# Optimization experiments

Measured on AMD Instinct MI355X. Metric: run time of the kernel, lower is better.

## Reference

```python
import jax, jax.numpy as jnp
import numpy as np


def setup_inputs() -> dict:
    key = jax.random.key(0)
    ks = jax.random.split(key, 8)
    N, C, H, W = 4, 128, 64, 64
    x = jax.random.normal(ks[0], (N, C, H, W), dtype=jnp.float32)
    s = 1.0 / np.sqrt(C)
    wq = jax.random.normal(ks[1], (C, C), dtype=jnp.float32) * s
    bq = jax.random.normal(ks[2], (C,), dtype=jnp.float32) * 0.01
    wk = jax.random.normal(ks[3], (C, C), dtype=jnp.float32) * s
    bk = jax.random.normal(ks[4], (C,), dtype=jnp.float32) * 0.01
    wv = jax.random.normal(ks[5], (C, C), dtype=jnp.float32) * s
    bv = jax.random.normal(ks[6], (C,), dtype=jnp.float32) * 0.01
    gamma = jax.random.normal(ks[7], (1,), dtype=jnp.float32) * 0.1
    return {"x": x, "wq": wq, "bq": bq, "wk": wk, "bk": bk,
            "wv": wv, "bv": bv, "gamma": gamma}


def reference(x, wq, bq, wk, bk, wv, bv, gamma):
    N, C, H, W = x.shape
    xf = x.reshape(N, C, H * W)                      # [N, C, HW]
    # 1x1 convs == per-pixel channel GEMMs
    q = jnp.einsum('dc,nci->ndi', wq, xf) + bq[None, :, None]  # [N, C, HW]
    k = jnp.einsum('dc,nci->ndi', wk, xf) + bk[None, :, None]
    v = jnp.einsum('dc,nci->ndi', wv, xf) + bv[None, :, None]
    # scores[n,i,j] = sum_c q[n,c,i] * k[n,c,j]  (query^T @ key)
    scores = jnp.einsum('nci,ncj->nij', q, k)        # [N, HW, HW]
    attn = jax.nn.softmax(scores, axis=-1)
    # out[n,c,i] = sum_j v[n,c,j] * attn[n,i,j]  (value @ attn^T)
    out = jnp.einsum('ncj,nij->nci', v, attn).reshape(N, C, H, W)
    return gamma[0] * out + x
```

## Files before the change

kernel.cpp:

```cpp
#include <hip/hip_runtime.h>

#define HW 4096
#define CC 128
#define NSPLIT 4
#define KEYS_PER_SPLIT (HW / NSPLIT)
#define LOG2E 1.44269504088896f

typedef __bf16 bf16x8 __attribute__((ext_vector_type(8)));
typedef __bf16 bf16x4 __attribute__((ext_vector_type(4)));
typedef __bf16 bf16x2 __attribute__((ext_vector_type(2)));
typedef float floatx4 __attribute__((ext_vector_type(4)));

__global__ __launch_bounds__(256) void wconv_kernel(
    const float* __restrict__ wq, const float* __restrict__ wk,
    const float* __restrict__ wv, __bf16* __restrict__ wb)
{
    int idx = blockIdx.x * 256 + threadIdx.x;
    int which = idx >> 14;
    int within = idx & 16383;
    const float* src = (which == 0) ? wq : (which == 1) ? wk : wv;
    wb[idx] = (__bf16)src[within];
}

#define XT_STRIDE 136
#define VT2_STRIDE 40

__global__ __launch_bounds__(256, 4) void proj_kernel(
    const float* __restrict__ x, const __bf16* __restrict__ wb,
    const float* __restrict__ bq, const float* __restrict__ bk,
    const float* __restrict__ bv,
    __bf16* __restrict__ qb, __bf16* __restrict__ kb, __bf16* __restrict__ vb)
{
    __shared__ char smem_raw[128 * VT2_STRIDE * 2];
    __bf16* Xt = reinterpret_cast<__bf16*>(smem_raw);
    __bf16* Vt = reinterpret_cast<__bf16*>(smem_raw);

    const int m   = blockIdx.x % 3;
    const int nit = blockIdx.x / 3;
    const int n   = nit >> 7;
    const int it  = nit & 127;
    const int i0  = it << 5;
    const int t   = threadIdx.x;

    const float* xb = x + (size_t)n * CC * HW;

    {
        const int f = t & 7;
        const int cb = t >> 3;
#pragma unroll
        for (int p = 0; p < 4; ++p) {
            int c = p * 32 + cb;
            float4 xv = *reinterpret_cast<const float4*>(&xb[(size_t)c * HW + i0 + f * 4]);
            Xt[(f * 4 + 0) * XT_STRIDE + c] = (__bf16)xv.x;
            Xt[(f * 4 + 1) * XT_STRIDE + c] = (__bf16)xv.y;
            Xt[(f * 4 + 2) * XT_STRIDE + c] = (__bf16)xv.z;
            Xt[(f * 4 + 3) * XT_STRIDE + c] = (__bf16)xv.w;
        }
    }
    __syncthreads();

    const int w    = t >> 6;
    const int lane = t & 63;
    const int l16  = lane & 15;
    const int quad = lane >> 4;
    const int d0   = w * 32;

    bf16x8 afrag[2][4];
#pragma unroll
    for (int it16 = 0; it16 < 2; ++it16)
#pragma unroll
        for (int ks = 0; ks < 4; ++ks)
            afrag[it16][ks] = *reinterpret_cast<const bf16x8*>(
                &Xt[(it16 * 16 + l16) * XT_STRIDE + ks * 32 + quad * 8]);

    const __bf16* wm = wb + (size_t)m * CC * CC;
    const float* Bm = (m == 0) ? bq : (m == 1) ? bk : bv;
    const float scale = (m == 0) ? LOG2E : 1.0f;

    floatx4 acc[2][2];
#pragma unroll
    for (int dt = 0; dt < 2; ++dt) {
        int d = d0 + dt * 16 + l16;
        bf16x8 bfrag[4];
#pragma unroll
        for (int ks = 0; ks < 4; ++ks)
            bfrag[ks] = *reinterpret_cast<const bf16x8*>(
                wm + (size_t)d * CC + ks * 32 + quad * 8);
#pragma unroll
        for (int it16 = 0; it16 < 2; ++it16) {
            acc[dt][it16] = (floatx4){0.f, 0.f, 0.f, 0.f};
#pragma unroll
            for (int ks = 0; ks < 4; ++ks)
                acc[dt][it16] = __builtin_amdgcn_mfma_f32_16x16x32_bf16(
                    afrag[it16][ks], bfrag[ks], acc[dt][it16], 0, 0, 0);
        }
    }

    if (m < 2) {
        __bf16* dst = (m == 0) ? qb : kb;
#pragma unroll
        for (int dt = 0; dt < 2; ++dt) {
            int d = d0 + dt * 16 + l16;
            float bias = Bm[d];
#pragma unroll
            for (int it16 = 0; it16 < 2; ++it16)
#pragma unroll
                for (int r = 0; r < 4; ++r) {
                    int i = i0 + it16 * 16 + quad * 4 + r;
                    dst[((size_t)n * HW + i) * CC + d] =
                        (__bf16)((acc[dt][it16][r] + bias) * scale);
                }
        }
    } else {
        __syncthreads();
#pragma unroll
        for (int dt = 0; dt < 2; ++dt) {
            int d = d0 + dt * 16 + l16;
            float bias = Bm[d];
#pragma unroll
            for (int it16 = 0; it16 < 2; ++it16)
#pragma unroll
                for (int r = 0; r < 4; ++r)
                    Vt[d * VT2_STRIDE + it16 * 16 + quad * 4 + r] =
                        (__bf16)(acc[dt][it16][r] + bias);
        }
        __syncthreads();
        {
            int d = t >> 1, half = t & 1;
            bf16x8 v0 = *reinterpret_cast<const bf16x8*>(&Vt[d * VT2_STRIDE + half * 16]);
            bf16x8 v1 = *reinterpret_cast<const bf16x8*>(&Vt[d * VT2_STRIDE + half * 16 + 8]);
            __bf16* vp = vb + ((size_t)n * CC + d) * HW + i0 + half * 16;
            *reinterpret_cast<bf16x8*>(vp)     = v0;
            *reinterpret_cast<bf16x8*>(vp + 8) = v1;
        }
    }
}

#define KT_STRIDE 136
#define KT_BYTES (64 * KT_STRIDE * 2)
#define VT_STRIDE 72
#define VT_BYTES (128 * VT_STRIDE * 2)
#define P_OFF    (KT_BYTES + VT_BYTES)
#define PT_STRIDE 72
#define PT_WAVE (32 * PT_STRIDE * 2)
#define T_STRIDE 65

__global__ __launch_bounds__(256, 2) void attn_split_kernel(
    const __bf16* __restrict__ qb, const __bf16* __restrict__ kb,
    const __bf16* __restrict__ vb,
    __bf16* __restrict__ opart, float* __restrict__ ml)
{
    __shared__ char smem[P_OFF + 4 * PT_WAVE];
    __bf16* Kt = reinterpret_cast<__bf16*>(smem);
    __bf16* Vt = reinterpret_cast<__bf16*>(smem + KT_BYTES);
    float*  T  = reinterpret_cast<float*>(smem);

    const int b     = blockIdx.x;
    const int n     = (b >> 1) & 3;
    const int split = (((b >> 3) & 1) << 1) | (b & 1);
    const int it    = b >> 4;
    const int i0    = it << 7;
    const int t     = threadIdx.x;
    const int w     = t >> 6;
    const int lane  = t & 63;
    const int l16   = lane & 15;
    const int quad  = lane >> 4;

    __bf16* Pt = reinterpret_cast<__bf16*>(smem + P_OFF) + w * (32 * PT_STRIDE);

    bf16x8 qfrag[2][4];
#pragma unroll
    for (int half = 0; half < 2; ++half) {
        const __bf16* qrow = qb + ((size_t)n * HW + i0 + w * 32 + half * 16 + l16) * CC;
#pragma unroll
        for (int ks = 0; ks < 4; ++ks)
            qfrag[half][ks] = *reinterpret_cast<const bf16x8*>(qrow + ks * 32 + quad * 8);
    }

    float m_i[2] = {-1e30f, -1e30f};
    float l_i[2] = {0.f, 0.f};
    floatx4 o_acc[2][8];
#pragma unroll
    for (int half = 0; half < 2; ++half)
#pragma unroll
        for (int h = 0; h < 8; ++h) o_acc[half][h] = (floatx4){0.f, 0.f, 0.f, 0.f};

    const __bf16* kbase = kb + (size_t)n * HW * CC;
    const __bf16* vbase = vb + (size_t)n * CC * HW;

    const int jbeg = split * KEYS_PER_SPLIT;
    const int jend = jbeg + KEYS_PER_SPLIT;

    const int jr = t >> 4, ch = t & 15;
    const int cv = t >> 3, ch2 = t & 7;

    for (int j0 = jbeg; j0 < jend; j0 += 64) {
        bf16x8 kst[4], vst[4];
#pragma unroll
        for (int p = 0; p < 4; ++p) {
            kst[p] = *reinterpret_cast<const bf16x8*>(
                kbase + (size_t)(j0 + p * 16 + jr) * CC + ch * 8);
            vst[p] = *reinterpret_cast<const bf16x8*>(
                vbase + (size_t)(p * 32 + cv) * HW + j0 + ch2 * 8);
        }
        __syncthreads();
#pragma unroll
        for (int p = 0; p < 4; ++p) {
            *reinterpret_cast<bf16x8*>(&Kt[(p * 16 + jr) * KT_STRIDE + ch * 8]) = kst[p];
            *reinterpret_cast<bf16x8*>(&Vt[(p * 32 + cv) * VT_STRIDE + ch2 * 8]) = vst[p];
        }
        __syncthreads();

        floatx4 s[2][4];
#pragma unroll
        for (int half = 0; half < 2; ++half)
#pragma unroll
            for (int g = 0; g < 4; ++g) s[half][g] = (floatx4){0.f, 0.f, 0.f, 0.f};
#pragma unroll
        for (int ks = 0; ks < 4; ++ks) {
#pragma unroll
            for (int g = 0; g < 4; ++g) {
                bf16x8 kf = *reinterpret_cast<const bf16x8*>(
                    &Kt[(g * 16 + l16) * KT_STRIDE + ks * 32 + quad * 8]);
                s[0][g] = __builtin_amdgcn_mfma_f32_16x16x32_bf16(kf, qfrag[0][ks], s[0][g], 0, 0, 0);
                s[1][g] = __builtin_amdgcn_mfma_f32_16x16x32_bf16(kf, qfrag[1][ks], s[1][g], 0, 0, 0);
            }
        }

#pragma unroll
        for (int half = 0; half < 2; ++half) {
            float rm = fmaxf(fmaxf(fmaxf(s[half][0][0], s[half][0][1]),
                                   fmaxf(s[half][0][2], s[half][0][3])),
                             fmaxf(fmaxf(s[half][1][0], s[half][1][1]),
                                   fmaxf(s[half][1][2], s[half][1][3])));
            float rm2 = fmaxf(fmaxf(fmaxf(s[half][2][0], s[half][2][1]),
                                    fmaxf(s[half][2][2], s[half][2][3])),
                              fmaxf(fmaxf(s[half][3][0], s[half][3][1]),
                                    fmaxf(s[half][3][2], s[half][3][3])));
            rm = fmaxf(rm, rm2);
            rm = fmaxf(rm, __shfl_xor(rm, 16, 64));
            rm = fmaxf(rm, __shfl_xor(rm, 32, 64));
            if (__any(rm > m_i[half])) {
                float mn = fmaxf(m_i[half], rm);
                float alpha = exp2f(m_i[half] - mn);
                m_i[half] = mn;
                l_i[half] *= alpha;
#pragma unroll
                for (int h = 0; h < 8; ++h)
                    o_acc[half][h] *= alpha;
            }
            float mi = m_i[half];
            float rs = 0.f;
#pragma unroll
            for (int g = 0; g < 4; ++g)
#pragma unroll
                for (int r = 0; r < 4; ++r) {
                    float e = exp2f(s[half][g][r] - mi);
                    s[half][g][r] = e;
                    rs += e;
                }
            rs += __shfl_xor(rs, 16, 64);
            rs += __shfl_xor(rs, 32, 64);
            l_i[half] += rs;

#pragma unroll
            for (int g = 0; g < 4; ++g) {
                bf16x4 pk = {(__bf16)s[half][g][0], (__bf16)s[half][g][1],
                             (__bf16)s[half][g][2], (__bf16)s[half][g][3]};
                *reinterpret_cast<bf16x4*>(
                    &Pt[(half * 16 + l16) * PT_STRIDE + g * 16 + quad * 4]) = pk;
            }
        }

#pragma unroll
        for (int tt = 0; tt < 2; ++tt) {
            bf16x8 pf0 = *reinterpret_cast<const bf16x8*>(
                &Pt[l16 * PT_STRIDE + tt * 32 + quad * 8]);
            bf16x8 pf1 = *reinterpret_cast<const bf16x8*>(
                &Pt[(16 + l16) * PT_STRIDE + tt * 32 + quad * 8]);
#pragma unroll
            for (int h = 0; h < 8; ++h) {
                bf16x8 vf = *reinterpret_cast<const bf16x8*>(
                    &Vt[(h * 16 + l16) * VT_STRIDE + tt * 32 + quad * 8]);
                o_acc[0][h] = __builtin_amdgcn_mfma_f32_16x16x32_bf16(vf, pf0, o_acc[0][h], 0, 0, 0);
                o_acc[1][h] = __builtin_amdgcn_mfma_f32_16x16x32_bf16(vf, pf1, o_acc[1][h], 0, 0, 0);
            }
        }
    }

    if (quad == 0) {
#pragma unroll
        for (int half = 0; half < 2; ++half) {
            int q = w * 32 + half * 16 + l16;
            ml[(size_t)b * 256 + q]       = m_i[half];
            ml[(size_t)b * 256 + 128 + q] = l_i[half];
        }
    }

    float inv[2] = {1.f / l_i[0], 1.f / l_i[1]};

    __syncthreads();
#pragma unroll
    for (int pass = 0; pass < 2; ++pass) {
        if ((w >> 1) == pass) {
            int ql = (w & 1) * 32;
#pragma unroll
            for (int half = 0; half < 2; ++half)
#pragma unroll
                for (int h = 0; h < 8; ++h)
#pragma unroll
                    for (int r = 0; r < 4; ++r)
                        T[(h * 16 + quad * 4 + r) * T_STRIDE + ql + half * 16 + l16] =
                            o_acc[half][h][r] * inv[half];
        }
        __syncthreads();
#pragma unroll 4
        for (int p = 0; p < 16; ++p) {
            int c  = p * 8 + (t >> 5);
            int q2 = (t & 31) * 2;
            float f0 = T[c * T_STRIDE + q2];
            float f1 = T[c * T_STRIDE + q2 + 1];
            bf16x2 pk = {(__bf16)f0, (__bf16)f1};
            *reinterpret_cast<bf16x2*>(
                &opart[(size_t)b * 16384 + (size_t)c * 128 + pass * 64 + q2]) = pk;
        }
        __syncthreads();
    }
}

__global__ __launch_bounds__(256) void combine_kernel(
    const __bf16* __restrict__ opart, const float* __restrict__ ml,
    const float* __restrict__ x, const float* __restrict__ gamma,
    float* __restrict__ out)
{
    __shared__ float wsc[NSPLIT][128];

    const int b2    = blockIdx.x;
    const int cpart = b2 & 7;
    const int qt    = b2 >> 3;
    const int n     = qt >> 5;
    const int it    = qt & 31;
    const int i0    = it << 7;
    const int t     = threadIdx.x;
    const float gm  = gamma[0];

    int battn[NSPLIT];
#pragma unroll
    for (int s = 0; s < NSPLIT; ++s)
        battn[s] = (it << 4) | ((s >> 1) << 3) | (n << 1) | (s & 1);

    if (t < 128) {
        float ms[NSPLIT], ls[NSPLIT], M = -1e30f;
#pragma unroll
        for (int s = 0; s < NSPLIT; ++s) {
            ms[s] = ml[(size_t)battn[s] * 256 + t];
            ls[s] = ml[(size_t)battn[s] * 256 + 128 + t];
            M = fmaxf(M, ms[s]);
        }
        float denom = 0.f, es[NSPLIT];
#pragma unroll
        for (int s = 0; s < NSPLIT; ++s) {
            es[s] = exp2f(ms[s] - M);
            denom += es[s] * ls[s];
        }
        float inv = gm / denom;
#pragma unroll
        for (int s = 0; s < NSPLIT; ++s)
            wsc[s][t] = es[s] * inv;
    }
    __syncthreads();

#pragma unroll
    for (int p = 0; p < 4; ++p) {
        int c  = cpart * 16 + p * 4 + (t >> 6);
        int q2 = (t & 63) * 2;
        size_t gidx = ((size_t)n * CC + c) * HW + i0 + q2;
        float2 xv = *reinterpret_cast<const float2*>(&x[gidx]);
        float a0 = xv.x, a1 = xv.y;
#pragma unroll
        for (int s = 0; s < NSPLIT; ++s) {
            bf16x2 ov = *reinterpret_cast<const bf16x2*>(
                &opart[(size_t)battn[s] * 16384 + (size_t)c * 128 + q2]);
            a0 += wsc[s][q2]     * (float)ov[0];
            a1 += wsc[s][q2 + 1] * (float)ov[1];
        }
        float2 o2 = {a0, a1};
        *reinterpret_cast<float2*>(&out[gidx]) = o2;
    }
}

extern "C" void kernel_launch(void* const* d_in, const int* in_sizes, int n_in,
                              void* d_out, int out_size, void* d_ws, size_t ws_size,
                              hipStream_t stream) {
    const float* x     = (const float*)d_in[0];
    const float* wq    = (const float*)d_in[1];
    const float* bq    = (const float*)d_in[2];
    const float* wk    = (const float*)d_in[3];
    const float* bk    = (const float*)d_in[4];
    const float* wv    = (const float*)d_in[5];
    const float* bv    = (const float*)d_in[6];
    const float* gamma = (const float*)d_in[7];
    float* out = (float*)d_out;

    char* ws = (char*)d_ws;
    const size_t qkv_sz = (size_t)4 * HW * CC * sizeof(__bf16);
    __bf16* qb = (__bf16*)(ws);
    __bf16* kb = (__bf16*)(ws + qkv_sz);
    __bf16* vb = (__bf16*)(ws + 2 * qkv_sz);
    __bf16* wb = (__bf16*)(ws + 3 * qkv_sz);
    __bf16* opart = (__bf16*)(ws + 3 * qkv_sz + 3 * CC * CC * sizeof(__bf16));
    float* ml = (float*)((char*)opart + (size_t)512 * 16384 * sizeof(__bf16));

    wconv_kernel<<<192, 256, 0, stream>>>(wq, wk, wv, wb);
    proj_kernel<<<1536, 256, 0, stream>>>(x, wb, bq, bk, bv, qb, kb, vb);
    attn_split_kernel<<<512, 256, 0, stream>>>(qb, kb, vb, opart, ml);
    combine_kernel<<<1024, 256, 0, stream>>>(opart, ml, x, gamma, out);
}
```

Measured before the change: 144.6 us.

## Stage K/V tiles via direct global-to-LDS DMA with double-buffered V and XOR swizzle

The attention loop now copies K and V tiles straight from global memory into LDS with global_load_lds, so they no longer pass through registers. V is double-buffered and K is prefetched once the score MFMAs finish, which overlaps the loads of the next tile with compute on the current one. Padded LDS strides are replaced by XOR-swizzled layouts for K, V and the per-wave P tile to avoid bank conflicts. The risk is that the DMA path needs correct swizzle and synchronisation, and the K prefetch can still stall on the barrier placed mid-iteration.

```diff
diff --git a/kernel.cpp b/kernel.cpp
--- a/kernel.cpp
+++ b/kernel.cpp
@@ -3,13 +3,21 @@
 #define HW 4096
 #define CC 128
 #define NSPLIT 4
-#define KEYS_PER_SPLIT (HW / NSPLIT)
+#define KPS (HW / NSPLIT)
+#define NJ (KPS / 64)
 #define LOG2E 1.44269504088896f
 
 typedef __bf16 bf16x8 __attribute__((ext_vector_type(8)));
 typedef __bf16 bf16x4 __attribute__((ext_vector_type(4)));
 typedef __bf16 bf16x2 __attribute__((ext_vector_type(2)));
 typedef float floatx4 __attribute__((ext_vector_type(4)));
+
+#define AS1 __attribute__((address_space(1)))
+#define AS3 __attribute__((address_space(3)))
+
+__device__ __forceinline__ void dma16(const __bf16* g, char* l) {
+    __builtin_amdgcn_global_load_lds((const AS1 void*)g, (AS3 void*)l, 16, 0, 0);
+}
 
 __global__ __launch_bounds__(256) void wconv_kernel(
     const float* __restrict__ wq, const float* __restrict__ wk,
@@ -38,19 +46,17 @@
     const int m   = blockIdx.x % 3;
     const int nit = blockIdx.x / 3;
     const int n   = nit >> 7;
-    const int it  = nit & 127;
-    const int i0  = it << 5;
+    const int i0  = (nit & 127) << 5;
     const int t   = threadIdx.x;
 
     const float* xb = x + (size_t)n * CC * HW;
 
     {
-        const int f = t & 7;
-        const int cb = t >> 3;
+        const int f = t & 7, cb = t >> 3;
 #pragma unroll
         for (int p = 0; p < 4; ++p) {
             int c = p * 32 + cb;
-            float4 xv = *reinterpret_cast<const float4*>(&xb[(size_t)c * HW + i0 + f * 4]);
+            float4 xv = *(const float4*)(&xb[(size_t)c * HW + i0 + f * 4]);
             Xt[(f * 4 + 0) * XT_STRIDE + c] = (__bf16)xv.x;
             Xt[(f * 4 + 1) * XT_STRIDE + c] = (__bf16)xv.y;
             Xt[(f * 4 + 2) * XT_STRIDE + c] = (__bf16)xv.z;
@@ -70,7 +76,7 @@
     for (int it16 = 0; it16 < 2; ++it16)
 #pragma unroll
         for (int ks = 0; ks < 4; ++ks)
-            afrag[it16][ks] = *reinterpret_cast<const bf16x8*>(
+            afrag[it16][ks] = *(const bf16x8*)(
                 &Xt[(it16 * 16 + l16) * XT_STRIDE + ks * 32 + quad * 8]);
 
     const __bf16* wm = wb + (size_t)m * CC * CC;
@@ -84,8 +90,7 @@
         bf16x8 bfrag[4];
 #pragma unroll
         for (int ks = 0; ks < 4; ++ks)
-            bfrag[ks] = *reinterpret_cast<const bf16x8*>(
-                wm + (size_t)d * CC + ks * 32 + quad * 8);
+            bfrag[ks] = *(const bf16x8*)(wm + (size_t)d * CC + ks * 32 + quad * 8);
 #pragma unroll
         for (int it16 = 0; it16 < 2; ++it16) {
             acc[dt][it16] = (floatx4){0.f, 0.f, 0.f, 0.f};
@@ -127,54 +132,50 @@
         __syncthreads();
         {
             int d = t >> 1, half = t & 1;
-            bf16x8 v0 = *reinterpret_cast<const bf16x8*>(&Vt[d * VT2_STRIDE + half * 16]);
-            bf16x8 v1 = *reinterpret_cast<const bf16x8*>(&Vt[d * VT2_STRIDE + half * 16 + 8]);
+            bf16x8 v0 = *(const bf16x8*)(&Vt[d * VT2_STRIDE + half * 16]);
+            bf16x8 v1 = *(const bf16x8*)(&Vt[d * VT2_STRIDE + half * 16 + 8]);
             __bf16* vp = vb + ((size_t)n * CC + d) * HW + i0 + half * 16;
-            *reinterpret_cast<bf16x8*>(vp)     = v0;
-            *reinterpret_cast<bf16x8*>(vp + 8) = v1;
-        }
-    }
-}
-
-#define KT_STRIDE 136
-#define KT_BYTES (64 * KT_STRIDE * 2)
-#define VT_STRIDE 72
-#define VT_BYTES (128 * VT_STRIDE * 2)
-#define P_OFF    (KT_BYTES + VT_BYTES)
-#define PT_STRIDE 72
-#define PT_WAVE (32 * PT_STRIDE * 2)
-#define T_STRIDE 65
+            *(bf16x8*)vp = v0;
+            *(bf16x8*)(vp + 8) = v1;
+        }
+    }
+}
+
+#define SMEM_BYTES 57344
+#define VT_OFF 16384
+#define P_OFF  49152
 
 __global__ __launch_bounds__(256, 2) void attn_split_kernel(
     const __bf16* __restrict__ qb, const __bf16* __restrict__ kb,
     const __bf16* __restrict__ vb,
     __bf16* __restrict__ opart, float* __restrict__ ml)
 {
-    __shared__ char smem[P_OFF + 4 * PT_WAVE];
-    __bf16* Kt = reinterpret_cast<__bf16*>(smem);
-    __bf16* Vt = reinterpret_cast<__bf16*>(smem + KT_BYTES);
-    float*  T  = reinterpret_cast<float*>(smem);
+    __shared__ __align__(16) char smem[SMEM_BYTES];
 
     const int b     = blockIdx.x;
     const int n     = (b >> 1) & 3;
     const int split = (((b >> 3) & 1) << 1) | (b & 1);
-    const int it    = b >> 4;
-    const int i0    = it << 7;
+    const int itq   = b >> 4;
+    const int i0    = itq << 7;
     const int t     = threadIdx.x;
     const int w     = t >> 6;
     const int lane  = t & 63;
     const int l16   = lane & 15;
     const int quad  = lane >> 4;
 
-    __bf16* Pt = reinterpret_cast<__bf16*>(smem + P_OFF) + w * (32 * PT_STRIDE);
+    char* Pw = smem + P_OFF + w * 2048;
+
+    const int jbeg = split * KPS;
+    const __bf16* kpane = kb + ((size_t)n * HW + jbeg) * CC;
+    const __bf16* vpane = vb + (size_t)n * CC * HW + jbeg;
 
     bf16x8 qfrag[2][4];
 #pragma unroll
     for (int half = 0; half < 2; ++half) {
-        const __bf16* qrow = qb + ((size_t)n * HW + i0 + w * 32 + half * 16 + l16) * CC;
+        const __bf16* qr = qb + ((size_t)n * HW + i0 + w * 32 + half * 16 + l16) * CC;
 #pragma unroll
         for (int ks = 0; ks < 4; ++ks)
-            qfrag[half][ks] = *reinterpret_cast<const bf16x8*>(qrow + ks * 32 + quad * 8);
+            qfrag[half][ks] = *(const bf16x8*)(qr + ks * 32 + quad * 8);
     }
 
     float m_i[2] = {-1e30f, -1e30f};
@@ -185,107 +186,120 @@
 #pragma unroll
         for (int h = 0; h < 8; ++h) o_acc[half][h] = (floatx4){0.f, 0.f, 0.f, 0.f};
 
-    const __bf16* kbase = kb + (size_t)n * HW * CC;
-    const __bf16* vbase = vb + (size_t)n * CC * HW;
-
-    const int jbeg = split * KEYS_PER_SPLIT;
-    const int jend = jbeg + KEYS_PER_SPLIT;
-
-    const int jr = t >> 4, ch = t & 15;
-    const int cv = t >> 3, ch2 = t & 7;
-
-    for (int j0 = jbeg; j0 < jend; j0 += 64) {
-        bf16x8 kst[4], vst[4];
+    int kcol[4], vcol[2];
+#pragma unroll
+    for (int ks = 0; ks < 4; ++ks) kcol[ks] = ((ks * 4 + quad) ^ l16) * 8;
+#pragma unroll
+    for (int tt = 0; tt < 2; ++tt) vcol[tt] = ((tt * 4 + quad) ^ (l16 & 7)) * 8;
+
+    auto stageK = [&](int j0) {
 #pragma unroll
         for (int p = 0; p < 4; ++p) {
-            kst[p] = *reinterpret_cast<const bf16x8*>(
-                kbase + (size_t)(j0 + p * 16 + jr) * CC + ch * 8);
-            vst[p] = *reinterpret_cast<const bf16x8*>(
-                vbase + (size_t)(p * 32 + cv) * HW + j0 + ch2 * 8);
-        }
-        __syncthreads();
+            int krow  = p * 16 + (t >> 4);
+            int kgblk = (t & 15) ^ ((t >> 4) & 15);
+            dma16(kpane + (size_t)(j0 + krow) * CC + kgblk * 8,
+                  smem + p * 4096 + t * 16);
+        }
+    };
+    auto stageV = [&](int j0, int buf) {
+        char* vd = smem + VT_OFF + buf * 16384;
 #pragma unroll
         for (int p = 0; p < 4; ++p) {
-            *reinterpret_cast<bf16x8*>(&Kt[(p * 16 + jr) * KT_STRIDE + ch * 8]) = kst[p];
-            *reinterpret_cast<bf16x8*>(&Vt[(p * 32 + cv) * VT_STRIDE + ch2 * 8]) = vst[p];
-        }
-        __syncthreads();
+            int vrow  = p * 32 + (t >> 3);
+            int vgblk = (t & 7) ^ ((t >> 3) & 7);
+            dma16(vpane + (size_t)vrow * HW + j0 + vgblk * 8,
+                  vd + p * 4096 + t * 16);
+        }
+    };
+
+    stageK(0);
+    stageV(0, 0);
+    int cur = 0;
+
+    for (int jt = 0; jt < NJ; ++jt) {
+        __syncthreads();
+        if (jt + 1 < NJ) stageV((jt + 1) * 64, cur ^ 1);
+
+        const __bf16* Kc = (const __bf16*)smem;
 
         floatx4 s[2][4];
 #pragma unroll
-        for (int half = 0; half < 2; ++half)
-#pragma unroll
-            for (int g = 0; g < 4; ++g) s[half][g] = (floatx4){0.f, 0.f, 0.f, 0.f};
+        for (int hh = 0; hh < 2; ++hh)
+#pragma unroll
+            for (int g = 0; g < 4; ++g) s[hh][g] = (floatx4){0.f, 0.f, 0.f, 0.f};
 #pragma unroll
         for (int ks = 0; ks < 4; ++ks) {
 #pragma unroll
             for (int g = 0; g < 4; ++g) {
-                bf16x8 kf = *reinterpret_cast<const bf16x8*>(
-                    &Kt[(g * 16 + l16) * KT_STRIDE + ks * 32 + quad * 8]);
+                bf16x8 kf = *(const bf16x8*)(Kc + (g * 16 + l16) * 128 + kcol[ks]);
                 s[0][g] = __builtin_amdgcn_mfma_f32_16x16x32_bf16(kf, qfrag[0][ks], s[0][g], 0, 0, 0);
                 s[1][g] = __builtin_amdgcn_mfma_f32_16x16x32_bf16(kf, qfrag[1][ks], s[1][g], 0, 0, 0);
             }
         }
 
-#pragma unroll
-        for (int half = 0; half < 2; ++half) {
-            float rm = fmaxf(fmaxf(fmaxf(s[half][0][0], s[half][0][1]),
-                                   fmaxf(s[half][0][2], s[half][0][3])),
-                             fmaxf(fmaxf(s[half][1][0], s[half][1][1]),
-                                   fmaxf(s[half][1][2], s[half][1][3])));
-            float rm2 = fmaxf(fmaxf(fmaxf(s[half][2][0], s[half][2][1]),
-                                    fmaxf(s[half][2][2], s[half][2][3])),
-                              fmaxf(fmaxf(s[half][3][0], s[half][3][1]),
-                                    fmaxf(s[half][3][2], s[half][3][3])));
+        __syncthreads();
+        if (jt + 1 < NJ) stageK((jt + 1) * 64);
+
+        bf16x8 pf[2][2];
+#pragma unroll
+        for (int hh = 0; hh < 2; ++hh) {
+            float rm = fmaxf(fmaxf(fmaxf(s[hh][0][0], s[hh][0][1]),
+                                   fmaxf(s[hh][0][2], s[hh][0][3])),
+                             fmaxf(fmaxf(s[hh][1][0], s[hh][1][1]),
+                                   fmaxf(s[hh][1][2], s[hh][1][3])));
+            float rm2 = fmaxf(fmaxf(fmaxf(s[hh][2][0], s[hh][2][1]),
+                                    fmaxf(s[hh][2][2], s[hh][2][3])),
+                              fmaxf(fmaxf(s[hh][3][0], s[hh][3][1]),
+                                    fmaxf(s[hh][3][2], s[hh][3][3])));
             rm = fmaxf(rm, rm2);
             rm = fmaxf(rm, __shfl_xor(rm, 16, 64));
             rm = fmaxf(rm, __shfl_xor(rm, 32, 64));
-            if (__any(rm > m_i[half])) {
-                float mn = fmaxf(m_i[half], rm);
-                float alpha = exp2f(m_i[half] - mn);
-                m_i[half] = mn;
-                l_i[half] *= alpha;
-#pragma unroll
-                for (int h = 0; h < 8; ++h)
-                    o_acc[half][h] *= alpha;
+            if (__any(rm > m_i[hh])) {
+                float mn = fmaxf(m_i[hh], rm);
+                float alpha = exp2f(m_i[hh] - mn);
+                m_i[hh] = mn;
+                l_i[hh] *= alpha;
+#pragma unroll
+                for (int h = 0; h < 8; ++h) o_acc[hh][h] *= alpha;
             }
-            float mi = m_i[half];
-            float rs = 0.f;
+            float mi = m_i[hh], rs = 0.f;
 #pragma unroll
             for (int g = 0; g < 4; ++g)
 #pragma unroll
                 for (int r = 0; r < 4; ++r) {
-                    float e = exp2f(s[half][g][r] - mi);
-                    s[half][g][r] = e;
+                    float e = exp2f(s[hh][g][r] - mi);
+                    s[hh][g][r] = e;
                     rs += e;
                 }
             rs += __shfl_xor(rs, 16, 64);
             rs += __shfl_xor(rs, 32, 64);
-            l_i[half] += rs;
+            l_i[hh] += rs;
 
 #pragma unroll
             for (int g = 0; g < 4; ++g) {
-                bf16x4 pk = {(__bf16)s[half][g][0], (__bf16)s[half][g][1],
-                             (__bf16)s[half][g][2], (__bf16)s[half][g][3]};
-                *reinterpret_cast<bf16x4*>(
-                    &Pt[(half * 16 + l16) * PT_STRIDE + g * 16 + quad * 4]) = pk;
+                bf16x4 pk = {(__bf16)s[hh][g][0], (__bf16)s[hh][g][1],
+                             (__bf16)s[hh][g][2], (__bf16)s[hh][g][3]};
+                int lblk = (g * 2 + (quad >> 1)) ^ (l16 & 7);
+                *(bf16x4*)(Pw + l16 * 128 + lblk * 16 + (quad & 1) * 8) = pk;
             }
-        }
-
+#pragma unroll
+            for (int tt = 0; tt < 2; ++tt) {
+                int rblk = (tt * 4 + quad) ^ (l16 & 7);
+                pf[hh][tt] = *(const bf16x8*)(Pw + l16 * 128 + rblk * 16);
+            }
+        }
+
+        const __bf16* Vc = (const __bf16*)(smem + VT_OFF + cur * 16384);
 #pragma unroll
         for (int tt = 0; tt < 2; ++tt) {
-            bf16x8 pf0 = *reinterpret_cast<const bf16x8*>(
-                &Pt[l16 * PT_STRIDE + tt * 32 + quad * 8]);
-            bf16x8 pf1 = *reinterpret_cast<const bf16x8*>(
-                &Pt[(16 + l16) * PT_STRIDE + tt * 32 + quad * 8]);
 #pragma unroll
             for (int h = 0; h < 8; ++h) {
-                bf16x8 vf = *reinterpret_cast<const bf16x8*>(
-                    &Vt[(h * 16 + l16) * VT_STRIDE + tt * 32 + quad * 8]);
-                o_acc[0][h] = __builtin_amdgcn_mfma_f32_16x16x32_bf16(vf, pf0, o_acc[0][h], 0, 0, 0);
-                o_acc[1][h] = __builtin_amdgcn_mfma_f32_16x16x32_bf16(vf, pf1, o_acc[1][h], 0, 0, 0);
+                bf16x8 vf = *(const bf16x8*)(Vc + (h * 16 + l16) * 64 + vcol[tt]);
+                o_acc[0][h] = __builtin_amdgcn_mfma_f32_16x16x32_bf16(vf, pf[0][tt], o_acc[0][h], 0, 0, 0);
+                o_acc[1][h] = __builtin_amdgcn_mfma_f32_16x16x32_bf16(vf, pf[1][tt], o_acc[1][h], 0, 0, 0);
             }
         }
+        cur ^= 1;
     }
 
     if (quad == 0) {
@@ -296,10 +310,10 @@
             ml[(size_t)b * 256 + 128 + q] = l_i[half];
         }
     }
-
-    float inv[2] = {1.f / l_i[0], 1.f / l_i[1]};
+    float linv[2] = {1.f / l_i[0], 1.f / l_i[1]};
 
     __syncthreads();
+    float* T = (float*)smem;
 #pragma unroll
     for (int pass = 0; pass < 2; ++pass) {
         if ((w >> 1) == pass) {
@@ -310,19 +324,16 @@
                 for (int h = 0; h < 8; ++h)
 #pragma unroll
                     for (int r = 0; r < 4; ++r)
-                        T[(h * 16 + quad * 4 + r) * T_STRIDE + ql + half * 16 + l16] =
-                            o_acc[half][h][r] * inv[half];
+                        T[(h * 16 + quad * 4 + r) * 65 + ql + half * 16 + l16] =
+                            o_acc[half][h][r] * linv[half];
         }
         __syncthreads();
 #pragma unroll 4
         for (int p = 0; p < 16; ++p) {
             int c  = p * 8 + (t >> 5);
             int q2 = (t & 31) * 2;
-            float f0 = T[c * T_STRIDE + q2];
-            float f1 = T[c * T_STRIDE + q2 + 1];
-            bf16x2 pk = {(__bf16)f0, (__bf16)f1};
-            *reinterpret_cast<bf16x2*>(
-                &opart[(size_t)b * 16384 + (size_t)c * 128 + pass * 64 + q2]) = pk;
+            bf16x2 pk = {(__bf16)T[c * 65 + q2], (__bf16)T[c * 65 + q2 + 1]};
+            *(bf16x2*)(&opart[(size_t)b * 16384 + (size_t)c * 128 + pass * 64 + q2]) = pk;
         }
         __syncthreads();
     }
@@ -375,17 +386,18 @@
         int c  = cpart * 16 + p * 4 + (t >> 6);
         int q2 = (t & 63) * 2;
         size_t gidx = ((size_t)n * CC + c) * HW + i0 + q2;
-        float2 xv = *reinterpret_cast<const float2*>(&x[gidx]);
+        float2 xv = *(const float2*)(&x[gidx]);
         float a0 = xv.x, a1 = xv.y;
 #pragma unroll
         for (int s = 0; s < NSPLIT; ++s) {
-            bf16x2 ov = *reinterpret_cast<const bf16x2*>(
+            bf16x2 ov = *(const bf16x2*)(
                 &opart[(size_t)battn[s] * 16384 + (size_t)c * 128 + q2]);
             a0 += wsc[s][q2]     * (float)ov[0];
             a1 += wsc[s][q2 + 1] * (float)ov[1];
         }
-        float2 o2 = {a0, a1};
-        *reinterpret_cast<float2*>(&out[gidx]) = o2;
+        float2 o2;
+        o2.x = a0; o2.y = a1;
+        *(float2*)(&out[gidx]) = o2;
     }
 }
 
```

Result: no change. 142.8 us (-1.2%).
